# Kernel tuning notes

Measured on AMD Instinct MI355X. Metric: run time of the kernel, lower is better.

The kernel has to match this reference:

```python
import jax, jax.numpy as jnp
import numpy as np

TAU = 0.3  # default tau in selectCom_adap
K = 1      # hard-coded K in selectCom_adap

B, C, N, M = 8, 64, 2048, 2048


def setup_inputs() -> dict:
    key = jax.random.key(0)
    k1, k2, k3, k4 = jax.random.split(key, 4)
    return {
        "src_emb": jax.random.normal(k1, (B, C, N), dtype=jnp.float32),
        "tgt_emb": jax.random.normal(k2, (B, C, M), dtype=jnp.float32),
        "src": jax.random.normal(k3, (B, 3, N), dtype=jnp.float32),
        "tgt": jax.random.normal(k4, (B, 3, M), dtype=jnp.float32),
    }


def reference(src_emb, tgt_emb, src, tgt):
    # EPCOR eval path: selectCom_adap + get_sparse_w
    dtype = src_emb.dtype
    Np = src_emb.shape[2]
    Mp = tgt_emb.shape[2]
    tgt_K = int(Mp * TAU)
    src_K = int(Np * TAU)

    inner = jnp.einsum('bcn,bcm->bnm', src_emb, tgt_emb)
    xx = jnp.sum(src_emb * src_emb, axis=1)[:, :, None]   # [B,N,1]
    yy = jnp.sum(tgt_emb * tgt_emb, axis=1)[:, None, :]   # [B,1,M]
    pd = 2.0 * inner - xx - yy                             # [B,N,M]

    # column softmax and tgt outlier mask (smallest tgt_K column mass)
    scoresSoftCol = jax.nn.softmax(pd, axis=2)
    scoresColSum = jnp.sum(scoresSoftCol, axis=1)          # [B,M]
    col_thresh = -jax.lax.top_k(-scoresColSum, tgt_K)[0][:, -1]  # tgt_K-th smallest, [B]
    mask_tgt = (scoresColSum < col_thresh[:, None])[:, None, :]  # [B,1,M]

    # row softmax and src outlier mask (smallest src_K row mass)
    scoresSoftRow = jax.nn.softmax(pd, axis=1)
    scoresRowSum = jnp.sum(scoresSoftRow, axis=2)          # [B,N]
    row_thresh = -jax.lax.top_k(-scoresRowSum, src_K)[0][:, -1]  # [B]
    mask_src = (scoresRowSum < row_thresh[:, None])[:, :, None]  # [B,N,1]

    mask = jnp.logical_or(mask_src, mask_tgt)              # [B,N,M]

    # torch precedence: mask = (mask + scoresSoftCol) < topk  (bool promoted to float)
    topk = jax.lax.top_k(scoresSoftCol, K)[0][..., -1:]    # K-th largest per row, [B,N,1]
    mask = (mask.astype(dtype) + scoresSoftCol) < topk     # [B,N,M]

    w_sparse = jnp.where(mask, jnp.zeros((), dtype), scoresSoftCol)
    colsum = jnp.sum(w_sparse, axis=-1, keepdims=True)
    colsum = jnp.where(colsum < 1e-5, jnp.asarray(1e-5, dtype), colsum)
    src_tgt_weight = w_sparse / colsum                     # row-renormalized sparse weights

    val_sum = jnp.sum(src_tgt_weight, axis=-1, keepdims=True)  # [B,N,1]
    val_sum_inlier = jnp.where(mask_src, jnp.zeros((), dtype), val_sum)[..., 0]  # [B,N]
    src_weight = val_sum_inlier / jnp.sum(val_sum_inlier, axis=-1, keepdims=True)

    # src_corr = tgt @ src_tgt_weight^T : [B,3,M] x [B,N,M] -> [B,3,N]
    src_corr = jnp.einsum('bdm,bnm->bdn', tgt, src_tgt_weight)
    return src_corr, src_weight, mask_src, mask_tgt
```

## Files before the change

kernel.cpp:

```cpp
#include <hip/hip_runtime.h>

#define BB 8
#define CC 64
#define NN 2048
#define MM 2048
#define KSEL 613
#define MT 32
#define MT2 16
#define NT2 16
#define NCH 16

#define OUT_W  (BB * 3 * NN)
#define OUT_MS (OUT_W + BB * NN)
#define OUT_MT (OUT_MS + BB * NN)

typedef __bf16 bf16x8 __attribute__((ext_vector_type(8)));
typedef float f32x4 __attribute__((ext_vector_type(4)));
typedef unsigned short u16;

#define MFMA16 __builtin_amdgcn_mfma_f32_16x16x32_bf16

__device__ __forceinline__ void split3(float a, u16& u0, u16& u1, u16& u2) {
    __bf16 h0 = (__bf16)a; float f0 = (float)h0;
    float r1 = a - f0;
    __bf16 h1 = (__bf16)r1; float f1 = (float)h1;
    float r2 = r1 - f1;
    __bf16 h2 = (__bf16)r2;
    u0 = __builtin_bit_cast(u16, h0);
    u1 = __builtin_bit_cast(u16, h1);
    u2 = __builtin_bit_cast(u16, h2);
}

__global__ __launch_bounds__(256) void split_k(const float* __restrict__ E,
                                               float* __restrict__ sq,
                                               unsigned* __restrict__ T0,
                                               unsigned* __restrict__ T1,
                                               unsigned* __restrict__ T2) {
    __shared__ float Ls[64][65];
    __shared__ float sacc[64];
    int b = blockIdx.y, n0 = blockIdx.x * 64, t = threadIdx.x;
    const float* Eb = E + (size_t)b * CC * NN + n0;
#pragma unroll
    for (int i = 0; i < 4; ++i) {
        int idx = (i << 8) + t, c = idx >> 4, nq = idx & 15;
        float4 v = *(const float4*)(Eb + (size_t)c * NN + (nq << 2));
        Ls[c][nq * 4 + 0] = v.x; Ls[c][nq * 4 + 1] = v.y;
        Ls[c][nq * 4 + 2] = v.z; Ls[c][nq * 4 + 3] = v.w;
    }
    __syncthreads();
    int j = t & 31, nn = t >> 5;
#pragma unroll
    for (int p = 0; p < 8; ++p) {
        int n = (p << 3) + nn;
        float a = Ls[2 * j][n], c = Ls[2 * j + 1][n];
        float s = a * a + c * c;
#pragma unroll
        for (int d = 1; d < 32; d <<= 1) s += __shfl_xor(s, d);
        if (j == 0) sacc[n] = s;
        u16 a0, a1, a2, c0, c1, c2;
        split3(a, a0, a1, a2);
        split3(c, c0, c1, c2);
        size_t row = (size_t)(b * NN + n0 + n) * 32 + j;
        T0[row] = (unsigned)a0 | ((unsigned)c0 << 16);
        T1[row] = (unsigned)a1 | ((unsigned)c1 << 16);
        T2[row] = (unsigned)a2 | ((unsigned)c2 << 16);
    }
    __syncthreads();
    if (t < 64) sq[b * NN + n0 + t] = sacc[t];
}

#define LD8(P) (*(const bf16x8*)(const void*)(P))

__global__ __launch_bounds__(256, 3) void gemm_pd_k(
    const unsigned* __restrict__ A0, const unsigned* __restrict__ A1, const unsigned* __restrict__ A2,
    const unsigned* __restrict__ B0, const unsigned* __restrict__ B1, const unsigned* __restrict__ B2,
    const float* __restrict__ xx, const float* __restrict__ yy,
    float* __restrict__ pd,
    float* __restrict__ rpM, float* __restrict__ rpS,
    float* __restrict__ cpM, float* __restrict__ cpS) {
    __shared__ float rowm2[2][128], rows2[2][128];
    __shared__ float colm2[2][128], cols2[2][128];
    int flat = blockIdx.x + (blockIdx.y << 4) + (blockIdx.z << 8);
    int b = flat & 7, rest = flat >> 3;
    int mt = rest & 15, nt = rest >> 4;
    int n0 = nt << 7;
    int m0 = mt << 7;
    int t = threadIdx.x, lane = t & 63, w = t >> 6;
    int wn = w >> 1, wm = w & 1;
    int g = lane >> 4, q = lane & 15;

    size_t offA = ((size_t)(b * NN + n0 + wn * 64 + q) << 7) + (g << 4);
    size_t offB = ((size_t)(b * MM + m0 + wm * 64 + q) << 7) + (g << 4);
    const char* pA0 = (const char*)A0 + offA;
    const char* pA1 = (const char*)A1 + offA;
    const char* pA2 = (const char*)A2 + offA;
    const char* pB0 = (const char*)B0 + offB;
    const char* pB1 = (const char*)B1 + offB;
    const char* pB2 = (const char*)B2 + offB;

    f32x4 acc[4][4] = {};

#pragma unroll
    for (int kc = 0; kc < 2; ++kc) {
        int ko = kc << 6;
        bf16x8 a0[4], b0[4], ax[4], bx[4];
#pragma unroll
        for (int i = 0; i < 4; ++i) {
            a0[i] = LD8(pA0 + ko + i * 2048);
            b0[i] = LD8(pB0 + ko + i * 2048);
            ax[i] = LD8(pA1 + ko + i * 2048);
            bx[i] = LD8(pB1 + ko + i * 2048);
        }
#pragma unroll
        for (int mg = 0; mg < 4; ++mg)
#pragma unroll
            for (int ng = 0; ng < 4; ++ng)
                acc[ng][mg] = MFMA16(a0[ng], b0[mg], acc[ng][mg], 0, 0, 0);
#pragma unroll
        for (int mg = 0; mg < 4; ++mg)
#pragma unroll
            for (int ng = 0; ng < 4; ++ng)
                acc[ng][mg] = MFMA16(a0[ng], bx[mg], acc[ng][mg], 0, 0, 0);
#pragma unroll
        for (int mg = 0; mg < 4; ++mg)
#pragma unroll
            for (int ng = 0; ng < 4; ++ng)
                acc[ng][mg] = MFMA16(ax[ng], b0[mg], acc[ng][mg], 0, 0, 0);
#pragma unroll
        for (int mg = 0; mg < 4; ++mg)
#pragma unroll
            for (int ng = 0; ng < 4; ++ng)
                acc[ng][mg] = MFMA16(ax[ng], bx[mg], acc[ng][mg], 0, 0, 0);
#pragma unroll
        for (int i = 0; i < 4; ++i) {
            ax[i] = LD8(pA2 + ko + i * 2048);
            bx[i] = LD8(pB2 + ko + i * 2048);
        }
#pragma unroll
        for (int mg = 0; mg < 4; ++mg)
#pragma unroll
            for (int ng = 0; ng < 4; ++ng)
                acc[ng][mg] = MFMA16(a0[ng], bx[mg], acc[ng][mg], 0, 0, 0);
#pragma unroll
        for (int mg = 0; mg < 4; ++mg)
#pragma unroll
            for (int ng = 0; ng < 4; ++ng)
                acc[ng][mg] = MFMA16(ax[ng], b0[mg], acc[ng][mg], 0, 0, 0);
    }

    int nbase = n0 + wn * 64;
    int mbase = m0 + wm * 64;
    float xv[4][4];
#pragma unroll
    for (int ng = 0; ng < 4; ++ng)
#pragma unroll
        for (int r = 0; r < 4; ++r)
            xv[ng][r] = xx[b * NN + nbase + ng * 16 + g * 4 + r];
    float yv[4];
#pragma unroll
    for (int mg = 0; mg < 4; ++mg) yv[mg] = yy[b * MM + mbase + mg * 16 + q];

#pragma unroll
    for (int ng = 0; ng < 4; ++ng)
#pragma unroll
        for (int r = 0; r < 4; ++r) {
            float* prow = pd + ((size_t)(b * NN + nbase + ng * 16 + g * 4 + r)) * MM + mbase + q;
#pragma unroll
            for (int mg = 0; mg < 4; ++mg) {
                float o = 2.f * acc[ng][mg][r] - xv[ng][r] - yv[mg];
                acc[ng][mg][r] = o;
                prow[mg * 16] = o;
            }
        }

#pragma unroll
    for (int ng = 0; ng < 4; ++ng)
#pragma unroll
        for (int r = 0; r < 4; ++r) {
            float mx = fmaxf(fmaxf(acc[ng][0][r], acc[ng][1][r]),
                             fmaxf(acc[ng][2][r], acc[ng][3][r]));
#pragma unroll
            for (int d = 1; d < 16; d <<= 1) mx = fmaxf(mx, __shfl_xor(mx, d));
            float s = __expf(acc[ng][0][r] - mx) + __expf(acc[ng][1][r] - mx) +
                      __expf(acc[ng][2][r] - mx) + __expf(acc[ng][3][r] - mx);
#pragma unroll
            for (int d = 1; d < 16; d <<= 1) s += __shfl_xor(s, d);
            if (q == 0) {
                int nl = wn * 64 + ng * 16 + g * 4 + r;
                rowm2[wm][nl] = mx;
                rows2[wm][nl] = s;
            }
        }

#pragma unroll
    for (int mg = 0; mg < 4; ++mg) {
        float cx = -3.4e38f;
#pragma unroll
        for (int ng = 0; ng < 4; ++ng)
#pragma unroll
            for (int r = 0; r < 4; ++r) cx = fmaxf(cx, acc[ng][mg][r]);
        cx = fmaxf(cx, __shfl_xor(cx, 16));
        cx = fmaxf(cx, __shfl_xor(cx, 32));
        float cs = 0.f;
#pragma unroll
        for (int ng = 0; ng < 4; ++ng)
#pragma unroll
            for (int r = 0; r < 4; ++r) cs += __expf(acc[ng][mg][r] - cx);
        cs += __shfl_xor(cs, 16);
        cs += __shfl_xor(cs, 32);
        if (lane < 16) {
            int ml = wm * 64 + mg * 16 + q;
            colm2[wn][ml] = cx;
            cols2[wn][ml] = cs;
        }
    }
    __syncthreads();

    if (t < 128) {
        float ma = rowm2[0][t], mb = rowm2[1][t];
        float M = fmaxf(ma, mb);
        float S = rows2[0][t] * __expf(ma - M) + rows2[1][t] * __expf(mb - M);
        size_t base = ((size_t)(b * MT2 + mt)) * NN + n0 + t;
        rpM[base] = M;
        rpS[base] = S;
    } else {
        int m = t - 128;
        float ma = colm2[0][m], mb = colm2[1][m];
        float M = fmaxf(ma, mb);
        float S = cols2[0][m] * __expf(ma - M) + cols2[1][m] * __expf(mb - M);
        size_t base = ((size_t)(b * NT2 + nt)) * MM + m0 + m;
        cpM[base] = M;
        cpS[base] = S;
    }
}

__global__ __launch_bounds__(256) void comb_rc_k(const float* __restrict__ rpM,
                                                 const float* __restrict__ rpS,
                                                 const float* __restrict__ cpM,
                                                 const float* __restrict__ cpS,
                                                 float* __restrict__ rowmax,
                                                 float* __restrict__ rowsum,
                                                 float* __restrict__ colmax,
                                                 float* __restrict__ colsum) {
    int b = blockIdx.y, which = blockIdx.z;
    int i = blockIdx.x * 256 + threadIdx.x;
    const float* pM = which ? cpM : rpM;
    const float* pS = which ? cpS : rpS;
    float* oM = which ? colmax : rowmax;
    float* oS = which ? colsum : rowsum;
    float Mv = -3.4e38f;
#pragma unroll
    for (int k = 0; k < 16; ++k) Mv = fmaxf(Mv, pM[(size_t)(b * 16 + k) * 2048 + i]);
    float S = 0.f;
#pragma unroll
    for (int k = 0; k < 16; ++k) {
        size_t o = (size_t)(b * 16 + k) * 2048 + i;
        S += pS[o] * __expf(pM[o] - Mv);
    }
    oM[b * 2048 + i] = Mv;
    oS[b * 2048 + i] = S;
}

__global__ __launch_bounds__(256) void cross_k(const float* __restrict__ pd,
                                               const float* __restrict__ rowmax,
                                               const float* __restrict__ rowsum,
                                               const float* __restrict__ colmax,
                                               const float* __restrict__ colsum,
                                               float* __restrict__ sRowp,
                                               float* __restrict__ sColp) {
    __shared__ float rmx[128], rin[128];
    __shared__ float rowpart[128][65];
    __shared__ float colacc[4][64];
    int b = blockIdx.z, nc = blockIdx.y, mtile = blockIdx.x;
    int m0 = mtile << 6;
    int t = threadIdx.x, mL = t & 63, ng = t >> 6;
    if (t < 128) {
        int n = nc * 128 + t;
        rmx[t] = rowmax[b * NN + n];
        rin[t] = 1.f / rowsum[b * NN + n];
    }
    float cmv = colmax[b * MM + m0 + mL];
    float civ = 1.f / colsum[b * MM + m0 + mL];
    __syncthreads();
    const float* base = pd + ((size_t)(b * NN + nc * 128)) * MM + m0 + mL;
    float scp = 0.f;
#pragma unroll
    for (int i = 0; i < 32; ++i) {
        int nl = (i << 2) + ng;
        float v = base[(size_t)nl * MM];
        scp += __expf(v - rmx[nl]) * rin[nl];
        rowpart[nl][mL] = __expf(v - cmv) * civ;
    }
    colacc[ng][mL] = scp;
    __syncthreads();
    if (t < 128) {
        float s = 0.f;
#pragma unroll
        for (int c = 0; c < 64; ++c) s += rowpart[t][c];
        sRowp[((size_t)(b * MT + mtile)) * NN + nc * 128 + t] = s;
    } else if (t < 192) {
        int m = t - 128;
        sColp[((size_t)(b * NCH + nc)) * MM + m0 + m] =
            colacc[0][m] + colacc[1][m] + colacc[2][m] + colacc[3][m];
    }
}

__global__ __launch_bounds__(256) void comb_s_k(const float* __restrict__ sRowp,
                                                const float* __restrict__ sColp,
                                                float* __restrict__ sRow,
                                                float* __restrict__ sCol) {
    int b = blockIdx.y, which = blockIdx.z;
    int i = blockIdx.x * 256 + threadIdx.x;
    if (!which) {
        float s = 0.f;
#pragma unroll
        for (int k = 0; k < MT; ++k) s += sRowp[(size_t)(b * MT + k) * NN + i];
        sRow[b * NN + i] = s;
    } else {
        float s = 0.f;
#pragma unroll
        for (int k = 0; k < NCH; ++k) s += sColp[(size_t)(b * NCH + k) * MM + i];
        sCol[b * MM + i] = s;
    }
}

__global__ __launch_bounds__(64) void select_k(const float* __restrict__ sRow,
                                               const float* __restrict__ sCol,
                                               float* __restrict__ rth,
                                               float* __restrict__ cth) {
    int kind = blockIdx.x, b = blockIdx.y, t = threadIdx.x;
    const float* vals = (kind == 0) ? (sRow + b * NN) : (sCol + b * MM);
    float v[32];
#pragma unroll
    for (int i = 0; i < 32; ++i) v[i] = vals[t + (i << 6)];
    unsigned lo = 0u, hi = 0x7F800000u;
    while (lo < hi) {
        unsigned mid = lo + ((hi - lo) >> 1);
        float pv = __uint_as_float(mid);
        int c = 0;
#pragma unroll
        for (int i = 0; i < 32; ++i) c += (v[i] <= pv) ? 1 : 0;
#pragma unroll
        for (int off = 32; off > 0; off >>= 1) c += __shfl_down(c, off);
        c = __shfl(c, 0);
        if (c >= KSEL + 1) hi = mid; else lo = mid + 1;
    }
    if (t == 0) { if (kind == 0) rth[b] = __uint_as_float(lo); else cth[b] = __uint_as_float(lo); }
}

__global__ __launch_bounds__(256) void masks_k(const float* __restrict__ sRow,
                                               const float* __restrict__ sCol,
                                               const float* __restrict__ rth,
                                               const float* __restrict__ cth,
                                               float* __restrict__ out) {
    int b = blockIdx.x, t = threadIdx.x;
    float r = rth[b], c = cth[b];
    int cnt = 0;
    bool ms[8];
#pragma unroll
    for (int i = 0; i < 8; ++i) {
        int n = t + (i << 8);
        ms[i] = sRow[b * NN + n] < r;
        out[OUT_MS + b * NN + n] = ms[i] ? 1.f : 0.f;
        out[OUT_MT + b * MM + n] = (sCol[b * MM + n] < c) ? 1.f : 0.f;
        cnt += ms[i] ? 0 : 1;
    }
#pragma unroll
    for (int off = 32; off > 0; off >>= 1) cnt += __shfl_down(cnt, off);
    __shared__ int wcnt[4];
    int wave = t >> 6, lane = t & 63;
    if (lane == 0) wcnt[wave] = cnt;
    __syncthreads();
    float inv = 1.f / (float)(wcnt[0] + wcnt[1] + wcnt[2] + wcnt[3]);
#pragma unroll
    for (int i = 0; i < 8; ++i) {
        int n = t + (i << 8);
        out[OUT_W + b * NN + n] = ms[i] ? 0.f : inv;
    }
}

__global__ __launch_bounds__(256) void corr_k(const float* __restrict__ pd,
                                              const float* __restrict__ rowmax,
                                              const float* __restrict__ rowsum,
                                              const float* __restrict__ sRow,
                                              const float* __restrict__ sCol,
                                              const float* __restrict__ rth,
                                              const float* __restrict__ cth,
                                              const float* __restrict__ tgt,
                                              float* __restrict__ out) {
    int b = blockIdx.y, n = blockIdx.x, t = threadIdx.x;
    const float4* row4 = (const float4*)(pd + ((size_t)b * NN + n) * MM);
    const float4* sc4 = (const float4*)(sCol + b * MM);
    const float4* tg4 = (const float4*)(tgt + (size_t)b * 3 * MM);
    float rmax = rowmax[b * NN + n];
    float rsum = rowsum[b * NN + n];
    float cthv = cth[b];
    bool msrc = sRow[b * NN + n] < rth[b];
    float cs = 0.f, d0 = 0.f, d1 = 0.f, d2 = 0.f;
#pragma unroll
    for (int g = 0; g < 2; ++g) {
        int j = t + (g << 8);
        float p[4], sc[4], t0[4], t1[4], t2[4];
        *(float4*)p = row4[j];
        *(float4*)sc = sc4[j];
        *(float4*)t0 = tg4[j];
        *(float4*)t1 = tg4[j + MM / 4];
        *(float4*)t2 = tg4[j + MM / 2];
#pragma unroll
        for (int c = 0; c < 4; ++c) {
            bool keep = msrc || (sc[c] < cthv) || (p[c] == rmax);
            if (keep) {
                float s = __expf(p[c] - rmax) / rsum;
                cs += s;
                d0 += s * t0[c];
                d1 += s * t1[c];
                d2 += s * t2[c];
            }
        }
    }
#pragma unroll
    for (int off = 32; off > 0; off >>= 1) {
        cs += __shfl_down(cs, off);
        d0 += __shfl_down(d0, off);
        d1 += __shfl_down(d1, off);
        d2 += __shfl_down(d2, off);
    }
    __shared__ float red[4][4];
    int wave = t >> 6, lane = t & 63;
    if (lane == 0) { red[wave][0] = cs; red[wave][1] = d0; red[wave][2] = d1; red[wave][3] = d2; }
    __syncthreads();
    if (t == 0) {
        float cT = red[0][0] + red[1][0] + red[2][0] + red[3][0];
        float e0 = red[0][1] + red[1][1] + red[2][1] + red[3][1];
        float e1 = red[0][2] + red[1][2] + red[2][2] + red[3][2];
        float e2 = red[0][3] + red[1][3] + red[2][3] + red[3][3];
        cT = (cT < 1e-5f) ? 1e-5f : cT;
        out[(b * 3 + 0) * NN + n] = e0 / cT;
        out[(b * 3 + 1) * NN + n] = e1 / cT;
        out[(b * 3 + 2) * NN + n] = e2 / cT;
    }
}

extern "C" void kernel_launch(void* const* d_in, const int* in_sizes, int n_in,
                              void* d_out, int out_size, void* d_ws, size_t ws_size,
                              hipStream_t stream) {
    const float* src_emb = (const float*)d_in[0];
    const float* tgt_emb = (const float*)d_in[1];
    const float* tgt = (const float*)d_in[3];
    float* out = (float*)d_out;

    float* ws = (float*)d_ws;
    float* pd     = ws;
    float* xx     = pd + (size_t)BB * NN * MM;
    float* yy     = xx + BB * NN;
    float* rowmax = yy + BB * MM;
    float* rowsum = rowmax + BB * NN;
    float* colmax = rowsum + BB * NN;
    float* colsum = colmax + BB * MM;
    float* sRow   = colsum + BB * MM;
    float* sCol   = sRow + BB * NN;
    float* rth    = sCol + BB * MM;
    float* cth    = rth + BB;
    float* rpM    = cth + BB;
    float* rpS    = rpM + (size_t)BB * 16 * NN;
    float* cpM    = rpS + (size_t)BB * 16 * NN;
    float* cpS    = cpM + (size_t)BB * 16 * MM;
    float* sRowp  = cpS + (size_t)BB * 16 * MM;
    float* sColp  = sRowp + (size_t)BB * MT * NN;
    unsigned* At0 = (unsigned*)(sColp + (size_t)BB * NCH * MM);
    unsigned* At1 = At0 + (size_t)BB * NN * 32;
    unsigned* At2 = At1 + (size_t)BB * NN * 32;
    unsigned* Bt0 = At2 + (size_t)BB * NN * 32;
    unsigned* Bt1 = Bt0 + (size_t)BB * MM * 32;
    unsigned* Bt2 = Bt1 + (size_t)BB * MM * 32;

    split_k<<<dim3(NN / 64, BB), 256, 0, stream>>>(src_emb, xx, At0, At1, At2);
    split_k<<<dim3(MM / 64, BB), 256, 0, stream>>>(tgt_emb, yy, Bt0, Bt1, Bt2);
    gemm_pd_k<<<dim3(MM / 128, NN / 128, BB), 256, 0, stream>>>(At0, At1, At2, Bt0, Bt1, Bt2,
                                                                xx, yy, pd, rpM, rpS, cpM, cpS);
    comb_rc_k<<<dim3(2048 / 256, BB, 2), 256, 0, stream>>>(rpM, rpS, cpM, cpS,
                                                           rowmax, rowsum, colmax, colsum);
    cross_k<<<dim3(MT, NCH, BB), 256, 0, stream>>>(pd, rowmax, rowsum, colmax, colsum, sRowp, sColp);
    comb_s_k<<<dim3(2048 / 256, BB, 2), 256, 0, stream>>>(sRowp, sColp, sRow, sCol);
    select_k<<<dim3(2, BB), 64, 0, stream>>>(sRow, sCol, rth, cth);
    masks_k<<<dim3(BB), 256, 0, stream>>>(sRow, sCol, rth, cth, out);
    corr_k<<<dim3(NN, BB), 256, 0, stream>>>(pd, rowmax, rowsum, sRow, sCol, rth, cth, tgt, out);
}
```

Baseline: 219.1 us.

## Recompute distance GEMM in each pass instead of materializing pd matrix

Drops the 128 MB pd buffer and recomputes the split-bf16 MFMA distance tile three times: once for row/column max and sum, once for the cross softmax sums, and once for the masked correspondence accumulation. The old cross and corr kernels each streamed pd from global memory; those passes now become compute-bound GEMM recomputations with fused epilogues. A new partial-sum buffer and a combine kernel produce the final correspondences. The cost is three times the MFMA work in exchange for removing roughly 384 MB of memory traffic.

```diff
diff --git a/kernel.cpp b/kernel.cpp
--- a/kernel.cpp
+++ b/kernel.cpp
@@ -5,10 +5,6 @@
 #define NN 2048
 #define MM 2048
 #define KSEL 613
-#define MT 32
-#define MT2 16
-#define NT2 16
-#define NCH 16
 
 #define OUT_W  (BB * 3 * NN)
 #define OUT_MS (OUT_W + BB * NN)
@@ -71,35 +67,10 @@
 
 #define LD8(P) (*(const bf16x8*)(const void*)(P))
 
-__global__ __launch_bounds__(256, 3) void gemm_pd_k(
-    const unsigned* __restrict__ A0, const unsigned* __restrict__ A1, const unsigned* __restrict__ A2,
-    const unsigned* __restrict__ B0, const unsigned* __restrict__ B1, const unsigned* __restrict__ B2,
-    const float* __restrict__ xx, const float* __restrict__ yy,
-    float* __restrict__ pd,
-    float* __restrict__ rpM, float* __restrict__ rpS,
-    float* __restrict__ cpM, float* __restrict__ cpS) {
-    __shared__ float rowm2[2][128], rows2[2][128];
-    __shared__ float colm2[2][128], cols2[2][128];
-    int flat = blockIdx.x + (blockIdx.y << 4) + (blockIdx.z << 8);
-    int b = flat & 7, rest = flat >> 3;
-    int mt = rest & 15, nt = rest >> 4;
-    int n0 = nt << 7;
-    int m0 = mt << 7;
-    int t = threadIdx.x, lane = t & 63, w = t >> 6;
-    int wn = w >> 1, wm = w & 1;
-    int g = lane >> 4, q = lane & 15;
-
-    size_t offA = ((size_t)(b * NN + n0 + wn * 64 + q) << 7) + (g << 4);
-    size_t offB = ((size_t)(b * MM + m0 + wm * 64 + q) << 7) + (g << 4);
-    const char* pA0 = (const char*)A0 + offA;
-    const char* pA1 = (const char*)A1 + offA;
-    const char* pA2 = (const char*)A2 + offA;
-    const char* pB0 = (const char*)B0 + offB;
-    const char* pB1 = (const char*)B1 + offB;
-    const char* pB2 = (const char*)B2 + offB;
-
-    f32x4 acc[4][4] = {};
-
+__device__ __forceinline__ void tile_core(
+    const char* pA0, const char* pA1, const char* pA2,
+    const char* pB0, const char* pB1, const char* pB2,
+    f32x4 (&acc)[4][4]) {
 #pragma unroll
     for (int kc = 0; kc < 2; ++kc) {
         int ko = kc << 6;
@@ -147,31 +118,46 @@
             for (int ng = 0; ng < 4; ++ng)
                 acc[ng][mg] = MFMA16(ax[ng], b0[mg], acc[ng][mg], 0, 0, 0);
     }
-
-    int nbase = n0 + wn * 64;
-    int mbase = m0 + wm * 64;
-    float xv[4][4];
-#pragma unroll
-    for (int ng = 0; ng < 4; ++ng)
-#pragma unroll
-        for (int r = 0; r < 4; ++r)
-            xv[ng][r] = xx[b * NN + nbase + ng * 16 + g * 4 + r];
-    float yv[4];
-#pragma unroll
-    for (int mg = 0; mg < 4; ++mg) yv[mg] = yy[b * MM + mbase + mg * 16 + q];
-
-#pragma unroll
-    for (int ng = 0; ng < 4; ++ng)
-#pragma unroll
-        for (int r = 0; r < 4; ++r) {
-            float* prow = pd + ((size_t)(b * NN + nbase + ng * 16 + g * 4 + r)) * MM + mbase + q;
-#pragma unroll
-            for (int mg = 0; mg < 4; ++mg) {
-                float o = 2.f * acc[ng][mg][r] - xv[ng][r] - yv[mg];
-                acc[ng][mg][r] = o;
-                prow[mg * 16] = o;
-            }
-        }
+}
+
+#define TILE_PROLOGUE                                                                  \
+    int flat = blockIdx.x + (blockIdx.y << 4) + (blockIdx.z << 8);                     \
+    int b = flat & 7, rest = flat >> 3;                                                \
+    int mt = rest & 15, nt = rest >> 4;                                                \
+    int n0 = nt << 7, m0 = mt << 7;                                                    \
+    int t = threadIdx.x, lane = t & 63, w = t >> 6;                                    \
+    int wn = w >> 1, wm = w & 1;                                                       \
+    int g = lane >> 4, q = lane & 15;                                                  \
+    size_t offA = ((size_t)(b * NN + n0 + wn * 64 + q) << 7) + (g << 4);               \
+    size_t offB = ((size_t)(b * MM + m0 + wm * 64 + q) << 7) + (g << 4);               \
+    f32x4 acc[4][4] = {};                                                              \
+    tile_core((const char*)A0 + offA, (const char*)A1 + offA, (const char*)A2 + offA,  \
+              (const char*)B0 + offB, (const char*)B1 + offB, (const char*)B2 + offB,  \
+              acc);                                                                    \
+    int nbase = n0 + wn * 64;                                                          \
+    int mbase = m0 + wm * 64;                                                          \
+    {                                                                                  \
+        float xv_[4][4], yv_[4];                                                       \
+        _Pragma("unroll") for (int ng = 0; ng < 4; ++ng)                               \
+            _Pragma("unroll") for (int r = 0; r < 4; ++r)                              \
+                xv_[ng][r] = xx[b * NN + nbase + ng * 16 + g * 4 + r];                 \
+        _Pragma("unroll") for (int mg = 0; mg < 4; ++mg)                               \
+            yv_[mg] = yy[b * MM + mbase + mg * 16 + q];                                \
+        _Pragma("unroll") for (int ng = 0; ng < 4; ++ng)                               \
+            _Pragma("unroll") for (int r = 0; r < 4; ++r)                              \
+                _Pragma("unroll") for (int mg = 0; mg < 4; ++mg)                       \
+                    acc[ng][mg][r] = 2.f * acc[ng][mg][r] - xv_[ng][r] - yv_[mg];      \
+    }
+
+__global__ __launch_bounds__(256, 4) void gemmA_k(
+    const unsigned* __restrict__ A0, const unsigned* __restrict__ A1, const unsigned* __restrict__ A2,
+    const unsigned* __restrict__ B0, const unsigned* __restrict__ B1, const unsigned* __restrict__ B2,
+    const float* __restrict__ xx, const float* __restrict__ yy,
+    float* __restrict__ rpM, float* __restrict__ rpS,
+    float* __restrict__ cpM, float* __restrict__ cpS) {
+    __shared__ float rowm2[2][128], rows2[2][128];
+    __shared__ float colm2[2][128], cols2[2][128];
+    TILE_PROLOGUE
 
 #pragma unroll
     for (int ng = 0; ng < 4; ++ng)
@@ -220,7 +206,7 @@
         float ma = rowm2[0][t], mb = rowm2[1][t];
         float M = fmaxf(ma, mb);
         float S = rows2[0][t] * __expf(ma - M) + rows2[1][t] * __expf(mb - M);
-        size_t base = ((size_t)(b * MT2 + mt)) * NN + n0 + t;
+        size_t base = ((size_t)(b * 16 + mt)) * NN + n0 + t;
         rpM[base] = M;
         rpS[base] = S;
     } else {
@@ -228,9 +214,140 @@
         float ma = colm2[0][m], mb = colm2[1][m];
         float M = fmaxf(ma, mb);
         float S = cols2[0][m] * __expf(ma - M) + cols2[1][m] * __expf(mb - M);
-        size_t base = ((size_t)(b * NT2 + nt)) * MM + m0 + m;
+        size_t base = ((size_t)(b * 16 + nt)) * MM + m0 + m;
         cpM[base] = M;
         cpS[base] = S;
+    }
+}
+
+__global__ __launch_bounds__(256, 4) void gemmB_k(
+    const unsigned* __restrict__ A0, const unsigned* __restrict__ A1, const unsigned* __restrict__ A2,
+    const unsigned* __restrict__ B0, const unsigned* __restrict__ B1, const unsigned* __restrict__ B2,
+    const float* __restrict__ xx, const float* __restrict__ yy,
+    const float* __restrict__ rowmax, const float* __restrict__ rowsum,
+    const float* __restrict__ colmax, const float* __restrict__ colsum,
+    float* __restrict__ sRowp,
+    float* __restrict__ sColp) {
+    __shared__ float rowS[2][128], colS[2][128];
+    TILE_PROLOGUE
+
+    float rmv[4][4], riv[4][4];
+#pragma unroll
+    for (int ng = 0; ng < 4; ++ng)
+#pragma unroll
+        for (int r = 0; r < 4; ++r) {
+            int n = nbase + ng * 16 + g * 4 + r;
+            rmv[ng][r] = rowmax[b * NN + n];
+            riv[ng][r] = 1.f / rowsum[b * NN + n];
+        }
+    float cmv[4], civ[4];
+#pragma unroll
+    for (int mg = 0; mg < 4; ++mg) {
+        int m = mbase + mg * 16 + q;
+        cmv[mg] = colmax[b * MM + m];
+        civ[mg] = 1.f / colsum[b * MM + m];
+    }
+
+#pragma unroll
+    for (int mg = 0; mg < 4; ++mg) {
+        float scp = 0.f;
+#pragma unroll
+        for (int ng = 0; ng < 4; ++ng)
+#pragma unroll
+            for (int r = 0; r < 4; ++r)
+                scp += __expf(acc[ng][mg][r] - rmv[ng][r]) * riv[ng][r];
+        scp += __shfl_xor(scp, 16);
+        scp += __shfl_xor(scp, 32);
+        if (lane < 16) colS[wn][wm * 64 + mg * 16 + q] = scp;
+    }
+
+#pragma unroll
+    for (int ng = 0; ng < 4; ++ng)
+#pragma unroll
+        for (int r = 0; r < 4; ++r) {
+            float srp = __expf(acc[ng][0][r] - cmv[0]) * civ[0] +
+                        __expf(acc[ng][1][r] - cmv[1]) * civ[1] +
+                        __expf(acc[ng][2][r] - cmv[2]) * civ[2] +
+                        __expf(acc[ng][3][r] - cmv[3]) * civ[3];
+#pragma unroll
+            for (int d = 1; d < 16; d <<= 1) srp += __shfl_xor(srp, d);
+            if (q == 0) rowS[wm][wn * 64 + ng * 16 + g * 4 + r] = srp;
+        }
+    __syncthreads();
+
+    if (t < 128) {
+        sRowp[((size_t)(b * 16 + mt)) * NN + n0 + t] = rowS[0][t] + rowS[1][t];
+    } else {
+        int m = t - 128;
+        sColp[((size_t)(b * 16 + nt)) * MM + m0 + m] = colS[0][m] + colS[1][m];
+    }
+}
+
+__global__ __launch_bounds__(256, 3) void gemmC_k(
+    const unsigned* __restrict__ A0, const unsigned* __restrict__ A1, const unsigned* __restrict__ A2,
+    const unsigned* __restrict__ B0, const unsigned* __restrict__ B1, const unsigned* __restrict__ B2,
+    const float* __restrict__ xx, const float* __restrict__ yy,
+    const float* __restrict__ rowmax, const float* __restrict__ rowsum,
+    const float* __restrict__ sRow, const float* __restrict__ sCol,
+    const float* __restrict__ rth, const float* __restrict__ cth,
+    const float* __restrict__ tgt,
+    float* __restrict__ corrP) {
+    __shared__ float cred[2][128][4];
+    TILE_PROLOGUE
+
+    float cthv = cth[b], rthv = rth[b];
+    float tg0[4], tg1[4], tg2[4];
+    bool mtg[4];
+#pragma unroll
+    for (int mg = 0; mg < 4; ++mg) {
+        int m = mbase + mg * 16 + q;
+        const float* tb = tgt + (size_t)b * 3 * MM + m;
+        tg0[mg] = tb[0]; tg1[mg] = tb[MM]; tg2[mg] = tb[2 * MM];
+        mtg[mg] = sCol[b * MM + m] < cthv;
+    }
+
+#pragma unroll
+    for (int ng = 0; ng < 4; ++ng)
+#pragma unroll
+        for (int r = 0; r < 4; ++r) {
+            int n = nbase + ng * 16 + g * 4 + r;
+            float rm = rowmax[b * NN + n];
+            float ri = 1.f / rowsum[b * NN + n];
+            bool msrc = sRow[b * NN + n] < rthv;
+            float cs = 0.f, d0 = 0.f, d1 = 0.f, d2 = 0.f;
+#pragma unroll
+            for (int mg = 0; mg < 4; ++mg) {
+                float o = acc[ng][mg][r];
+                bool keep = msrc || mtg[mg] || (o == rm);
+                if (keep) {
+                    float s = __expf(o - rm) * ri;
+                    cs += s;
+                    d0 += s * tg0[mg];
+                    d1 += s * tg1[mg];
+                    d2 += s * tg2[mg];
+                }
+            }
+#pragma unroll
+            for (int d = 1; d < 16; d <<= 1) {
+                cs += __shfl_xor(cs, d);
+                d0 += __shfl_xor(d0, d);
+                d1 += __shfl_xor(d1, d);
+                d2 += __shfl_xor(d2, d);
+            }
+            if (q == 0) {
+                int nl = wn * 64 + ng * 16 + g * 4 + r;
+                cred[wm][nl][0] = cs; cred[wm][nl][1] = d0;
+                cred[wm][nl][2] = d1; cred[wm][nl][3] = d2;
+            }
+        }
+    __syncthreads();
+
+    if (t < 128) {
+        size_t base = ((size_t)(b * 16 + mt) * 4) * NN + n0 + t;
+        corrP[base]          = cred[0][t][0] + cred[1][t][0];
+        corrP[base + NN]     = cred[0][t][1] + cred[1][t][1];
+        corrP[base + 2 * NN] = cred[0][t][2] + cred[1][t][2];
+        corrP[base + 3 * NN] = cred[0][t][3] + cred[1][t][3];
     }
 }
 
@@ -261,50 +378,6 @@
     oS[b * 2048 + i] = S;
 }
 
-__global__ __launch_bounds__(256) void cross_k(const float* __restrict__ pd,
-                                               const float* __restrict__ rowmax,
-                                               const float* __restrict__ rowsum,
-                                               const float* __restrict__ colmax,
-                                               const float* __restrict__ colsum,
-                                               float* __restrict__ sRowp,
-                                               float* __restrict__ sColp) {
-    __shared__ float rmx[128], rin[128];
-    __shared__ float rowpart[128][65];
-    __shared__ float colacc[4][64];
-    int b = blockIdx.z, nc = blockIdx.y, mtile = blockIdx.x;
-    int m0 = mtile << 6;
-    int t = threadIdx.x, mL = t & 63, ng = t >> 6;
-    if (t < 128) {
-        int n = nc * 128 + t;
-        rmx[t] = rowmax[b * NN + n];
-        rin[t] = 1.f / rowsum[b * NN + n];
-    }
-    float cmv = colmax[b * MM + m0 + mL];
-    float civ = 1.f / colsum[b * MM + m0 + mL];
-    __syncthreads();
-    const float* base = pd + ((size_t)(b * NN + nc * 128)) * MM + m0 + mL;
-    float scp = 0.f;
-#pragma unroll
-    for (int i = 0; i < 32; ++i) {
-        int nl = (i << 2) + ng;
-        float v = base[(size_t)nl * MM];
-        scp += __expf(v - rmx[nl]) * rin[nl];
-        rowpart[nl][mL] = __expf(v - cmv) * civ;
-    }
-    colacc[ng][mL] = scp;
-    __syncthreads();
-    if (t < 128) {
-        float s = 0.f;
-#pragma unroll
-        for (int c = 0; c < 64; ++c) s += rowpart[t][c];
-        sRowp[((size_t)(b * MT + mtile)) * NN + nc * 128 + t] = s;
-    } else if (t < 192) {
-        int m = t - 128;
-        sColp[((size_t)(b * NCH + nc)) * MM + m0 + m] =
-            colacc[0][m] + colacc[1][m] + colacc[2][m] + colacc[3][m];
-    }
-}
-
 __global__ __launch_bounds__(256) void comb_s_k(const float* __restrict__ sRowp,
                                                 const float* __restrict__ sColp,
                                                 float* __restrict__ sRow,
@@ -314,14 +387,33 @@
     if (!which) {
         float s = 0.f;
 #pragma unroll
-        for (int k = 0; k < MT; ++k) s += sRowp[(size_t)(b * MT + k) * NN + i];
+        for (int k = 0; k < 16; ++k) s += sRowp[(size_t)(b * 16 + k) * NN + i];
         sRow[b * NN + i] = s;
     } else {
         float s = 0.f;
 #pragma unroll
-        for (int k = 0; k < NCH; ++k) s += sColp[(size_t)(b * NCH + k) * MM + i];
+        for (int k = 0; k < 16; ++k) s += sColp[(size_t)(b * 16 + k) * MM + i];
         sCol[b * MM + i] = s;
     }
+}
+
+__global__ __launch_bounds__(256) void comb_corr_k(const float* __restrict__ corrP,
+                                                   float* __restrict__ out) {
+    int b = blockIdx.y;
+    int i = blockIdx.x * 256 + threadIdx.x;
+    float cs = 0.f, d0 = 0.f, d1 = 0.f, d2 = 0.f;
+#pragma unroll
+    for (int k = 0; k < 16; ++k) {
+        size_t base = ((size_t)(b * 16 + k) * 4) * NN + i;
+        cs += corrP[base];
+        d0 += corrP[base + NN];
+        d1 += corrP[base + 2 * NN];
+        d2 += corrP[base + 3 * NN];
+    }
+    cs = (cs < 1e-5f) ? 1e-5f : cs;
+    out[(b * 3 + 0) * NN + i] = d0 / cs;
+    out[(b * 3 + 1) * NN + i] = d1 / cs;
+    out[(b * 3 + 2) * NN + i] = d2 / cs;
 }
 
 __global__ __launch_bounds__(64) void select_k(const float* __restrict__ sRow,
@@ -379,68 +471,6 @@
     }
 }
 
-__global__ __launch_bounds__(256) void corr_k(const float* __restrict__ pd,
-                                              const float* __restrict__ rowmax,
-                                              const float* __restrict__ rowsum,
-                                              const float* __restrict__ sRow,
-                                              const float* __restrict__ sCol,
-                                              const float* __restrict__ rth,
-                                              const float* __restrict__ cth,
-                                              const float* __restrict__ tgt,
-                                              float* __restrict__ out) {
-    int b = blockIdx.y, n = blockIdx.x, t = threadIdx.x;
-    const float4* row4 = (const float4*)(pd + ((size_t)b * NN + n) * MM);
-    const float4* sc4 = (const float4*)(sCol + b * MM);
-    const float4* tg4 = (const float4*)(tgt + (size_t)b * 3 * MM);
-    float rmax = rowmax[b * NN + n];
-    float rsum = rowsum[b * NN + n];
-    float cthv = cth[b];
-    bool msrc = sRow[b * NN + n] < rth[b];
-    float cs = 0.f, d0 = 0.f, d1 = 0.f, d2 = 0.f;
-#pragma unroll
-    for (int g = 0; g < 2; ++g) {
-        int j = t + (g << 8);
-        float p[4], sc[4], t0[4], t1[4], t2[4];
-        *(float4*)p = row4[j];
-        *(float4*)sc = sc4[j];
-        *(float4*)t0 = tg4[j];
-        *(float4*)t1 = tg4[j + MM / 4];
-        *(float4*)t2 = tg4[j + MM / 2];
-#pragma unroll
-        for (int c = 0; c < 4; ++c) {
-            bool keep = msrc || (sc[c] < cthv) || (p[c] == rmax);
-            if (keep) {
-                float s = __expf(p[c] - rmax) / rsum;
-                cs += s;
-                d0 += s * t0[c];
-                d1 += s * t1[c];
-                d2 += s * t2[c];
-            }
-        }
-    }
-#pragma unroll
-    for (int off = 32; off > 0; off >>= 1) {
-        cs += __shfl_down(cs, off);
-        d0 += __shfl_down(d0, off);
-        d1 += __shfl_down(d1, off);
-        d2 += __shfl_down(d2, off);
-    }
-    __shared__ float red[4][4];
-    int wave = t >> 6, lane = t & 63;
-    if (lane == 0) { red[wave][0] = cs; red[wave][1] = d0; red[wave][2] = d1; red[wave][3] = d2; }
-    __syncthreads();
-    if (t == 0) {
-        float cT = red[0][0] + red[1][0] + red[2][0] + red[3][0];
-        float e0 = red[0][1] + red[1][1] + red[2][1] + red[3][1];
-        float e1 = red[0][2] + red[1][2] + red[2][2] + red[3][2];
-        float e2 = red[0][3] + red[1][3] + red[2][3] + red[3][3];
-        cT = (cT < 1e-5f) ? 1e-5f : cT;
-        out[(b * 3 + 0) * NN + n] = e0 / cT;
-        out[(b * 3 + 1) * NN + n] = e1 / cT;
-        out[(b * 3 + 2) * NN + n] = e2 / cT;
-    }
-}
-
 extern "C" void kernel_launch(void* const* d_in, const int* in_sizes, int n_in,
                               void* d_out, int out_size, void* d_ws, size_t ws_size,
                               hipStream_t stream) {
@@ -450,8 +480,7 @@
     float* out = (float*)d_out;
 
     float* ws = (float*)d_ws;
-    float* pd     = ws;
-    float* xx     = pd + (size_t)BB * NN * MM;
+    float* xx     = ws;
     float* yy     = xx + BB * NN;
     float* rowmax = yy + BB * MM;
     float* rowsum = rowmax + BB * NN;
@@ -466,23 +495,31 @@
     float* cpM    = rpS + (size_t)BB * 16 * NN;
     float* cpS    = cpM + (size_t)BB * 16 * MM;
     float* sRowp  = cpS + (size_t)BB * 16 * MM;
-    float* sColp  = sRowp + (size_t)BB * MT * NN;
-    unsigned* At0 = (unsigned*)(sColp + (size_t)BB * NCH * MM);
+    float* sColp  = sRowp + (size_t)BB * 16 * NN;
+    float* corrP  = sColp + (size_t)BB * 16 * MM;
+    unsigned* At0 = (unsigned*)(corrP + (size_t)BB * 16 * 4 * NN);
     unsigned* At1 = At0 + (size_t)BB * NN * 32;
     unsigned* At2 = At1 + (size_t)BB * NN * 32;
     unsigned* Bt0 = At2 + (size_t)BB * NN * 32;
     unsigned* Bt1 = Bt0 + (size_t)BB * MM * 32;
     unsigned* Bt2 = Bt1 + (size_t)BB * MM * 32;
 
+    dim3 gemm_grid(16, 16, BB);
+
     split_k<<<dim3(NN / 64, BB), 256, 0, stream>>>(src_emb, xx, At0, At1, At2);
     split_k<<<dim3(MM / 64, BB), 256, 0, stream>>>(tgt_emb, yy, Bt0, Bt1, Bt2);
-    gemm_pd_k<<<dim3(MM / 128, NN / 128, BB), 256, 0, stream>>>(At0, At1, At2, Bt0, Bt1, Bt2,
-                                                                xx, yy, pd, rpM, rpS, cpM, cpS);
+    gemmA_k<<<gemm_grid, 256, 0, stream>>>(At0, At1, At2, Bt0, Bt1, Bt2,
+                                           xx, yy, rpM, rpS, cpM, cpS);
     comb_rc_k<<<dim3(2048 / 256, BB, 2), 256, 0, stream>>>(rpM, rpS, cpM, cpS,
                                                            rowmax, rowsum, colmax, colsum);
-    cross_k<<<dim3(MT, NCH, BB), 256, 0, stream>>>(pd, rowmax, rowsum, colmax, colsum, sRowp, sColp);
+    gemmB_k<<<gemm_grid, 256, 0, stream>>>(At0, At1, At2, Bt0, Bt1, Bt2,
+                                           xx, yy, rowmax, rowsum, colmax, colsum,
+                                           sRowp, sColp);
     comb_s_k<<<dim3(2048 / 256, BB, 2), 256, 0, stream>>>(sRowp, sColp, sRow, sCol);
     select_k<<<dim3(2, BB), 64, 0, stream>>>(sRow, sCol, rth, cth);
     masks_k<<<dim3(BB), 256, 0, stream>>>(sRow, sCol, rth, cth, out);
-    corr_k<<<dim3(NN, BB), 256, 0, stream>>>(pd, rowmax, rowsum, sRow, sCol, rth, cth, tgt, out);
-}
+    gemmC_k<<<gemm_grid, 256, 0, stream>>>(At0, At1, At2, Bt0, Bt1, Bt2,
+                                           xx, yy, rowmax, rowsum, sRow, sCol,
+                                           rth, cth, tgt, corrP);
+    comb_corr_k<<<dim3(2048 / 256, BB), 256, 0, stream>>>(corrP, out);
+}
```

Result: slower. 302.9 us (+38.3%).
